# Performance work log

Hardware: AMD Instinct MI355X
Metric: run time of the kernel (lower is better)

## Reference

```python
import jax, jax.numpy as jnp
import numpy as np

B, N, D_IN = 4, 512, 64
D_ATT, D_HID, D_ATT_NUM = 32, 128, 2
A_HID = 64
MASK_CONST = 10000.0


def _mlp2(x, W1, b1, W2, b2):
    # 2-layer MLP (Linear-ReLU-Linear), as built by cfg_Block('mlp', ...)
    return jax.nn.relu(x @ W1 + b1) @ W2 + b2


def setup_inputs() -> dict:
    key = jax.random.key(0)
    ks = jax.random.split(key, 32)
    s = 0.1

    def w(k, shp):
        return (jax.random.normal(k, shp, dtype=jnp.float32) * s)

    inp = {"x": jax.random.normal(ks[0], (B, N, D_IN), dtype=jnp.float32)}
    # key / query / value encoders: 64 -> 128 -> 32
    for i, p in enumerate(["k", "q", "v"]):
        inp[p + "W1"] = w(ks[1 + 2 * i], (D_IN, D_HID)); inp[p + "b1"] = jnp.zeros((D_HID,), jnp.float32)
        inp[p + "W2"] = w(ks[2 + 2 * i], (D_HID, D_ATT)); inp[p + "b2"] = jnp.zeros((D_ATT,), jnp.float32)
    # attention MLP: 2*D_att -> 64 -> D_att_num
    inp["aW1"] = w(ks[7], (2 * D_ATT, A_HID)); inp["ab1"] = jnp.zeros((A_HID,), jnp.float32)
    inp["aW2"] = w(ks[8], (A_HID, D_ATT_NUM)); inp["ab2"] = jnp.zeros((D_ATT_NUM,), jnp.float32)
    # decoders (x and y): 2*D_att -> 128 -> 64, then mu/sig heads 64 -> 1
    for i, p in enumerate(["dx", "dy"]):
        inp[p + "W1"] = w(ks[9 + 2 * i], (2 * D_ATT, D_HID)); inp[p + "b1"] = jnp.zeros((D_HID,), jnp.float32)
        inp[p + "W2"] = w(ks[10 + 2 * i], (D_HID, A_HID)); inp[p + "b2"] = jnp.zeros((A_HID,), jnp.float32)
    for i, p in enumerate(["mx", "sx", "my", "sy"]):
        inp[p + "W"] = w(ks[13 + i], (A_HID, 1)); inp[p + "b"] = jnp.zeros((1,), jnp.float32)
    return inp


def reference(x, kW1, kb1, kW2, kb2, qW1, qb1, qW2, qb2, vW1, vb1, vW2, vb2,
              aW1, ab1, aW2, ab2, dxW1, dxb1, dxW2, dxb2, dyW1, dyb1, dyW2, dyb2,
              mxW, mxb, sxW, sxb, myW, myb, syW, syb):
    k = _mlp2(x, kW1, kb1, kW2, kb2)  # [B,N,D_att]
    q = _mlp2(x, qW1, qb1, qW2, qb2)
    v = _mlp2(x, vW1, vb1, vW2, vb2)

    # z[b,i,j] = cat(k[b,i], q[b,j]); first att layer applied without
    # materializing z: z@aW1 = k@aW1[:D] + q@aW1[D:]
    hk = k @ aW1[:D_ATT]          # [B,N,A_HID]
    hq = q @ aW1[D_ATT:]          # [B,N,A_HID]
    h = jax.nn.relu(hk[:, :, None, :] + hq[:, None, :, :] + ab1)  # [B,N,N,A_HID]
    score = h @ aW2 + ab2          # [B,N,N,D_att_num]

    mask = jnp.eye(N, dtype=x.dtype)[None, :, :, None] * MASK_CONST
    w = jax.nn.sigmoid(score - mask)  # [B,N,N,D_att_num]

    agg0 = jnp.einsum('bij,bjd->bid', w[..., 0], v)
    agg1 = jnp.einsum('bij,bjd->bid', w[..., 1], v)
    c0 = jnp.concatenate([v, agg0], axis=-1)  # [B,N,2*D_att]
    c1 = jnp.concatenate([v, agg1], axis=-1)

    d_x = _mlp2(c0, dxW1, dxb1, dxW2, dxb2)
    mu_x = jnp.squeeze(d_x @ mxW + mxb, -1)                 # [B,N]
    sig_x = jnp.squeeze(jax.nn.softplus(d_x @ sxW + sxb), -1)
    d_y = _mlp2(c1, dyW1, dyb1, dyW2, dyb2)
    mu_y = jnp.squeeze(d_y @ myW + myb, -1)
    sig_y = jnp.squeeze(jax.nn.softplus(d_y @ syW + syb), -1)
    return ((mu_x, sig_x), (mu_y, sig_y))
```

## Files before the change

kernel.cpp:

```cpp
#include <hip/hip_runtime.h>
#include <hip/hip_bf16.h>

#define BB 4
#define NN 512

#define WS_V    0
#define WS_HK   65536
#define WS_HQ   196608
#define WS_AGG  327680

__global__ __launch_bounds__(256) void k_enc(
    const float* __restrict__ x,
    const float* __restrict__ kW1, const float* __restrict__ kb1,
    const float* __restrict__ kW2, const float* __restrict__ kb2,
    const float* __restrict__ qW1, const float* __restrict__ qb1,
    const float* __restrict__ qW2, const float* __restrict__ qb2,
    const float* __restrict__ vW1, const float* __restrict__ vb1,
    const float* __restrict__ vW2, const float* __restrict__ vb2,
    const float* __restrict__ aW1, const float* __restrict__ ab1,
    float* __restrict__ wsf)
{
  const int t = threadIdx.x;
  const int bid = blockIdx.x;
  const int e  = bid >> 8;
  const int r0 = (bid & 255) * 8;

  __shared__ float xs[8][64];
  __shared__ float h1s[8][132];
  __shared__ float encs[8][33];

  const float* W1 = (e == 0) ? kW1 : (e == 1) ? qW1 : vW1;
  const float* b1 = (e == 0) ? kb1 : (e == 1) ? qb1 : vb1;
  const float* W2 = (e == 0) ? kW2 : (e == 1) ? qW2 : vW2;
  const float* b2 = (e == 0) ? kb2 : (e == 1) ? qb2 : vb2;

  {
    float2 f = ((const float2*)x)[(size_t)r0 * 32 + t];
    int m = t * 2;
    xs[m >> 6][m & 63] = f.x;
    xs[(m + 1) >> 6][(m + 1) & 63] = f.y;
  }
  __syncthreads();

  {
    const int h = t & 127, rh = t >> 7;
    float acc[4];
    float bb = b1[h];
    #pragma unroll
    for (int r = 0; r < 4; ++r) acc[r] = bb;
    #pragma unroll 4
    for (int i = 0; i < 64; ++i) {
      float wv = W1[i * 128 + h];
      #pragma unroll
      for (int r = 0; r < 4; ++r) acc[r] = fmaf(xs[rh * 4 + r][i], wv, acc[r]);
    }
    #pragma unroll
    for (int r = 0; r < 4; ++r) h1s[rh * 4 + r][h] = fmaxf(acc[r], 0.f);
  }
  __syncthreads();

  {
    const int row = t >> 5, c = t & 31;
    float a = b2[c];
    #pragma unroll 4
    for (int i = 0; i < 128; ++i)
      a = fmaf(h1s[row][i], W2[i * 32 + c], a);
    if (e == 2) wsf[WS_V + (size_t)(r0 + row) * 32 + c] = a;
    else        encs[row][c] = a;
  }

  if (e != 2) {
    __syncthreads();
    const int h = t & 63, rp = t >> 6;
    float bias = (e == 0) ? ab1[h] : 0.f;
    float s0 = bias, s1 = bias;
    const float* aw = aW1 + (e ? 32 * 64 : 0);
    #pragma unroll 4
    for (int cc = 0; cc < 32; ++cc) {
      float wv = aw[cc * 64 + h];
      s0 = fmaf(encs[rp * 2 + 0][cc], wv, s0);
      s1 = fmaf(encs[rp * 2 + 1][cc], wv, s1);
    }
    float* dst = wsf + (e ? WS_HQ : WS_HK);
    dst[(size_t)(r0 + rp * 2 + 0) * 64 + h] = s0;
    dst[(size_t)(r0 + rp * 2 + 1) * 64 + h] = s1;
  }
}

__global__ __launch_bounds__(256, 4) void k_att(
    const float* __restrict__ v_ws, const float* __restrict__ hk_ws,
    const float* __restrict__ hq_ws, const float* __restrict__ aW2,
    const float* __restrict__ ab2, float* __restrict__ aggh)
{
  const int t = threadIdx.x;
  const int bid = blockIdx.x;
  const int jq = bid & 3;
  const int it = (bid >> 2) & 127;
  const int b  = bid >> 9;
  const int i0 = it * 4;
  const int jbase = jq * 128;

  const int q   = t & 3;
  const int jj1 = (t >> 2) & 15;
  const int ii1 = t >> 6;
  const int ig  = i0 + ii1;

  const int dd  = t & 15;
  const int c2  = (t >> 4) & 1;
  const int jh  = (t >> 5) & 1;
  const int i2  = t >> 6;

  __shared__ float hqs[2][16][68];
  __shared__ float vs[2][16][36];
  __shared__ float ws_w[2][4][20];

  float hk16[16];
  {
    const float4* hkp = (const float4*)(hk_ws + ((size_t)b * NN + ig) * 64 + q * 16);
    #pragma unroll
    for (int m = 0; m < 4; ++m) {
      float4 f = hkp[m];
      hk16[4 * m] = f.x; hk16[4 * m + 1] = f.y;
      hk16[4 * m + 2] = f.z; hk16[4 * m + 3] = f.w;
    }
  }
  float aw0[16], aw1[16];
  {
    const float4* awp = (const float4*)(aW2 + q * 32);
    #pragma unroll
    for (int k = 0; k < 8; ++k) {
      float4 f = awp[k];
      aw0[2 * k] = f.x;     aw1[2 * k] = f.y;
      aw0[2 * k + 1] = f.z; aw1[2 * k + 1] = f.w;
    }
  }
  const float sb0 = ab2[0], sb1 = ab2[1];

  float accx = 0.f, accy = 0.f;
  const bool vload = (t < 128);

  {
    float4 hq_r = *(const float4*)(hq_ws + ((size_t)b * NN + jbase + (t >> 4)) * 64 + (t & 15) * 4);
    *(float4*)(&hqs[0][t >> 4][(t & 15) * 4]) = hq_r;
    if (vload) {
      float4 v_r = *(const float4*)(v_ws + ((size_t)b * NN + jbase + (t >> 3)) * 32 + (t & 7) * 4);
      *(float4*)(&vs[0][t >> 3][(t & 7) * 4]) = v_r;
    }
  }
  __syncthreads();

  int p = 0;
  for (int jt = 0; jt < 8; ++jt) {
    const int j0 = jbase + jt * 16;

    float4 hq_n, v_n;
    if (jt < 7) {
      const int j0n = j0 + 16;
      hq_n = *(const float4*)(hq_ws + ((size_t)b * NN + j0n + (t >> 4)) * 64 + (t & 15) * 4);
      if (vload)
        v_n = *(const float4*)(v_ws + ((size_t)b * NN + j0n + (t >> 3)) * 32 + (t & 7) * 4);
    }

    {
      float s0 = 0.f, s1 = 0.f;
      #pragma unroll
      for (int mc = 0; mc < 4; ++mc) {
        float4 hq4 = *(const float4*)(&hqs[p][jj1][q * 16 + mc * 4]);
        float z;
        z = fmaxf(hk16[4 * mc + 0] + hq4.x, 0.f);
        s0 = fmaf(z, aw0[4 * mc + 0], s0); s1 = fmaf(z, aw1[4 * mc + 0], s1);
        z = fmaxf(hk16[4 * mc + 1] + hq4.y, 0.f);
        s0 = fmaf(z, aw0[4 * mc + 1], s0); s1 = fmaf(z, aw1[4 * mc + 1], s1);
        z = fmaxf(hk16[4 * mc + 2] + hq4.z, 0.f);
        s0 = fmaf(z, aw0[4 * mc + 2], s0); s1 = fmaf(z, aw1[4 * mc + 2], s1);
        z = fmaxf(hk16[4 * mc + 3] + hq4.w, 0.f);
        s0 = fmaf(z, aw0[4 * mc + 3], s0); s1 = fmaf(z, aw1[4 * mc + 3], s1);
      }
      s0 += __shfl_xor(s0, 1); s0 += __shfl_xor(s0, 2);
      s1 += __shfl_xor(s1, 1); s1 += __shfl_xor(s1, 2);
      s0 += sb0; s1 += sb1;
      float sel = (q & 1) ? s1 : s0;
      float w = 1.f / (1.f + __expf(-sel));
      if (ig == j0 + jj1) w = 0.f;
      if (q < 2) ws_w[q][ii1][jj1] = w;
    }
    __syncthreads();

    {
      float4 w4a = *(const float4*)(&ws_w[c2][i2][jh * 8]);
      float4 w4b = *(const float4*)(&ws_w[c2][i2][jh * 8 + 4]);
      const int jb = jh * 8;
      float2 vv;
      vv = *(const float2*)(&vs[p][jb + 0][2 * dd]);
      accx = fmaf(w4a.x, vv.x, accx); accy = fmaf(w4a.x, vv.y, accy);
      vv = *(const float2*)(&vs[p][jb + 1][2 * dd]);
      accx = fmaf(w4a.y, vv.x, accx); accy = fmaf(w4a.y, vv.y, accy);
      vv = *(const float2*)(&vs[p][jb + 2][2 * dd]);
      accx = fmaf(w4a.z, vv.x, accx); accy = fmaf(w4a.z, vv.y, accy);
      vv = *(const float2*)(&vs[p][jb + 3][2 * dd]);
      accx = fmaf(w4a.w, vv.x, accx); accy = fmaf(w4a.w, vv.y, accy);
      vv = *(const float2*)(&vs[p][jb + 4][2 * dd]);
      accx = fmaf(w4b.x, vv.x, accx); accy = fmaf(w4b.x, vv.y, accy);
      vv = *(const float2*)(&vs[p][jb + 5][2 * dd]);
      accx = fmaf(w4b.y, vv.x, accx); accy = fmaf(w4b.y, vv.y, accy);
      vv = *(const float2*)(&vs[p][jb + 6][2 * dd]);
      accx = fmaf(w4b.z, vv.x, accx); accy = fmaf(w4b.z, vv.y, accy);
      vv = *(const float2*)(&vs[p][jb + 7][2 * dd]);
      accx = fmaf(w4b.w, vv.x, accx); accy = fmaf(w4b.w, vv.y, accy);
    }

    if (jt < 7) {
      *(float4*)(&hqs[p ^ 1][t >> 4][(t & 15) * 4]) = hq_n;
      if (vload) *(float4*)(&vs[p ^ 1][t >> 3][(t & 7) * 4]) = v_n;
    }
    __syncthreads();
    p ^= 1;
  }

  accx += __shfl_xor(accx, 32);
  accy += __shfl_xor(accy, 32);
  if (jh == 0) {
    const size_t row = (size_t)b * NN + i0 + i2;
    float2 o; o.x = accx; o.y = accy;
    *(float2*)(&aggh[((size_t)(c2 * 4 + jq) * 2048 + row) * 32 + 2 * dd]) = o;
  }
}

__global__ __launch_bounds__(256) void k_dec(
    const float* __restrict__ v_ws, const float* __restrict__ aggh,
    const float* __restrict__ dxW1, const float* __restrict__ dxb1,
    const float* __restrict__ dxW2, const float* __restrict__ dxb2,
    const float* __restrict__ dyW1, const float* __restrict__ dyb1,
    const float* __restrict__ dyW2, const float* __restrict__ dyb2,
    const float* __restrict__ mxW, const float* __restrict__ mxb,
    const float* __restrict__ sxW, const float* __restrict__ sxb,
    const float* __restrict__ myW, const float* __restrict__ myb,
    const float* __restrict__ syW, const float* __restrict__ syb,
    float* __restrict__ out)
{
  const int t = threadIdx.x;
  const int bid = blockIdx.x;
  const int half = bid & 1;
  const int r0 = (bid >> 1) * 2;

  __shared__ float ccs[2][64];
  __shared__ float h1s[2][132];
  __shared__ float dds[2][64];

  if (t < 128) {
    const float* aggp = aggh + (size_t)half * 4 * 65536;
    int r = t >> 6, i = t & 63;
    size_t row = (size_t)(r0 + r);
    float val;
    if (i < 32) {
      val = v_ws[row * 32 + i];
    } else {
      int o = i - 32;
      val = aggp[row * 32 + o] + aggp[65536 + row * 32 + o]
          + aggp[131072 + row * 32 + o] + aggp[196608 + row * 32 + o];
    }
    ccs[r][i] = val;
  }
  __syncthreads();

  const float* W1 = half ? dyW1 : dxW1;
  const float* b1 = half ? dyb1 : dxb1;
  const float* W2 = half ? dyW2 : dxW2;
  const float* b2 = half ? dyb2 : dxb2;

  {
    const int h = t & 127, r = t >> 7;
    float acc = b1[h];
    #pragma unroll 4
    for (int i = 0; i < 64; ++i)
      acc = fmaf(ccs[r][i], W1[i * 128 + h], acc);
    h1s[r][h] = fmaxf(acc, 0.f);
  }
  __syncthreads();

  if (t < 128) {
    const int r = t >> 6, c = t & 63;
    float a = b2[c];
    #pragma unroll 4
    for (int i = 0; i < 128; ++i)
      a = fmaf(h1s[r][i], W2[i * 64 + c], a);
    dds[r][c] = a;
  }
  __syncthreads();

  {
    const int w = t >> 6, lane = t & 63;
    if (w < 2) {
      const float* mW = half ? myW : mxW;
      const float* sW = half ? syW : sxW;
      const float* mb = half ? myb : mxb;
      const float* sb = half ? syb : sxb;
      float dval = dds[w][lane];
      float pm = dval * mW[lane], ps = dval * sW[lane];
      #pragma unroll
      for (int msk = 32; msk >= 1; msk >>= 1) {
        pm += __shfl_xor(pm, msk);
        ps += __shfl_xor(ps, msk);
      }
      if (lane == 0) {
        float mu = pm + mb[0];
        float z = ps + sb[0];
        float sp = (z > 20.f) ? z : log1pf(__expf(z));
        out[half * 4096 + (r0 + w)] = mu;
        out[half * 4096 + 2048 + (r0 + w)] = sp;
      }
    }
  }
}

extern "C" void kernel_launch(void* const* d_in, const int* in_sizes, int n_in,
                              void* d_out, int out_size, void* d_ws, size_t ws_size,
                              hipStream_t stream) {
  (void)in_sizes; (void)n_in; (void)out_size; (void)ws_size;
  const float* x   = (const float*)d_in[0];
  const float* kW1 = (const float*)d_in[1];  const float* kb1 = (const float*)d_in[2];
  const float* kW2 = (const float*)d_in[3];  const float* kb2 = (const float*)d_in[4];
  const float* qW1 = (const float*)d_in[5];  const float* qb1 = (const float*)d_in[6];
  const float* qW2 = (const float*)d_in[7];  const float* qb2 = (const float*)d_in[8];
  const float* vW1 = (const float*)d_in[9];  const float* vb1 = (const float*)d_in[10];
  const float* vW2 = (const float*)d_in[11]; const float* vb2 = (const float*)d_in[12];
  const float* aW1 = (const float*)d_in[13]; const float* ab1 = (const float*)d_in[14];
  const float* aW2 = (const float*)d_in[15]; const float* ab2 = (const float*)d_in[16];
  const float* dxW1 = (const float*)d_in[17]; const float* dxb1 = (const float*)d_in[18];
  const float* dxW2 = (const float*)d_in[19]; const float* dxb2 = (const float*)d_in[20];
  const float* dyW1 = (const float*)d_in[21]; const float* dyb1 = (const float*)d_in[22];
  const float* dyW2 = (const float*)d_in[23]; const float* dyb2 = (const float*)d_in[24];
  const float* mxW = (const float*)d_in[25]; const float* mxb = (const float*)d_in[26];
  const float* sxW = (const float*)d_in[27]; const float* sxb = (const float*)d_in[28];
  const float* myW = (const float*)d_in[29]; const float* myb = (const float*)d_in[30];
  const float* syW = (const float*)d_in[31]; const float* syb = (const float*)d_in[32];

  float* wsf = (float*)d_ws;
  float* out = (float*)d_out;

  hipLaunchKernelGGL(k_enc, dim3(768), dim3(256), 0, stream,
                     x, kW1, kb1, kW2, kb2, qW1, qb1, qW2, qb2, vW1, vb1, vW2, vb2,
                     aW1, ab1, wsf);
  hipLaunchKernelGGL(k_att, dim3(2048), dim3(256), 0, stream,
                     wsf + WS_V, wsf + WS_HK, wsf + WS_HQ, aW2, ab2,
                     wsf + WS_AGG);
  hipLaunchKernelGGL(k_dec, dim3(2048), dim3(256), 0, stream,
                     wsf + WS_V, wsf + WS_AGG,
                     dxW1, dxb1, dxW2, dxb2, dyW1, dyb1, dyW2, dyb2,
                     mxW, mxb, sxW, sxb, myW, myb, syW, syb, out);
}
```

Baseline: 175.0 us.

## Double j-tile width in attention and process four rows per decoder block

The attention kernel now splits j into two halves instead of four and handles 32 j per tile with two sub-iterations, so there are half as many blocks and barriers per j and half as many partial aggregates to write. The decoder now handles four rows per block, reusing each W1 load across two rows and using all threads. It sums two partials instead of four. Fewer blocks may reduce parallelism, and the larger tiles raise shared memory and register use.

```diff
diff --git a/kernel.cpp b/kernel.cpp
--- a/kernel.cpp
+++ b/kernel.cpp
@@ -94,14 +94,14 @@
 {
   const int t = threadIdx.x;
   const int bid = blockIdx.x;
-  const int jq = bid & 3;
-  const int it = (bid >> 2) & 127;
-  const int b  = bid >> 9;
+  const int jq = bid & 1;
+  const int it = (bid >> 1) & 127;
+  const int b  = bid >> 8;
   const int i0 = it * 4;
-  const int jbase = jq * 128;
+  const int jbase = jq * 256;
 
   const int q   = t & 3;
-  const int jj1 = (t >> 2) & 15;
+  const int jj0 = (t >> 2) & 15;
   const int ii1 = t >> 6;
   const int ig  = i0 + ii1;
 
@@ -110,9 +110,9 @@
   const int jh  = (t >> 5) & 1;
   const int i2  = t >> 6;
 
-  __shared__ float hqs[2][16][68];
-  __shared__ float vs[2][16][36];
-  __shared__ float ws_w[2][4][20];
+  __shared__ float hqs[2][32][68];
+  __shared__ float vs[2][32][36];
+  __shared__ float ws_w[2][4][36];
 
   float hk16[16];
   {
@@ -137,35 +137,39 @@
   const float sb0 = ab2[0], sb1 = ab2[1];
 
   float accx = 0.f, accy = 0.f;
-  const bool vload = (t < 128);
-
-  {
-    float4 hq_r = *(const float4*)(hq_ws + ((size_t)b * NN + jbase + (t >> 4)) * 64 + (t & 15) * 4);
-    *(float4*)(&hqs[0][t >> 4][(t & 15) * 4]) = hq_r;
-    if (vload) {
-      float4 v_r = *(const float4*)(v_ws + ((size_t)b * NN + jbase + (t >> 3)) * 32 + (t & 7) * 4);
-      *(float4*)(&vs[0][t >> 3][(t & 7) * 4]) = v_r;
-    }
+
+  const int hr0 = t >> 4, hc0 = (t & 15) * 4;
+  const int vr0 = t >> 3, vc0 = (t & 7) * 4;
+
+  {
+    float4 a = *(const float4*)(hq_ws + ((size_t)b * NN + jbase + hr0) * 64 + hc0);
+    float4 c = *(const float4*)(hq_ws + ((size_t)b * NN + jbase + 16 + hr0) * 64 + hc0);
+    float4 v = *(const float4*)(v_ws + ((size_t)b * NN + jbase + vr0) * 32 + vc0);
+    *(float4*)(&hqs[0][hr0][hc0]) = a;
+    *(float4*)(&hqs[0][16 + hr0][hc0]) = c;
+    *(float4*)(&vs[0][vr0][vc0]) = v;
   }
   __syncthreads();
 
   int p = 0;
   for (int jt = 0; jt < 8; ++jt) {
-    const int j0 = jbase + jt * 16;
-
-    float4 hq_n, v_n;
+    const int j0 = jbase + jt * 32;
+
+    float4 hq_n0, hq_n1, v_n;
     if (jt < 7) {
-      const int j0n = j0 + 16;
-      hq_n = *(const float4*)(hq_ws + ((size_t)b * NN + j0n + (t >> 4)) * 64 + (t & 15) * 4);
-      if (vload)
-        v_n = *(const float4*)(v_ws + ((size_t)b * NN + j0n + (t >> 3)) * 32 + (t & 7) * 4);
-    }
-
-    {
+      const int j0n = j0 + 32;
+      hq_n0 = *(const float4*)(hq_ws + ((size_t)b * NN + j0n + hr0) * 64 + hc0);
+      hq_n1 = *(const float4*)(hq_ws + ((size_t)b * NN + j0n + 16 + hr0) * 64 + hc0);
+      v_n   = *(const float4*)(v_ws + ((size_t)b * NN + j0n + vr0) * 32 + vc0);
+    }
+
+    #pragma unroll
+    for (int sub = 0; sub < 2; ++sub) {
+      const int jj = jj0 + sub * 16;
       float s0 = 0.f, s1 = 0.f;
       #pragma unroll
       for (int mc = 0; mc < 4; ++mc) {
-        float4 hq4 = *(const float4*)(&hqs[p][jj1][q * 16 + mc * 4]);
+        float4 hq4 = *(const float4*)(&hqs[p][jj][q * 16 + mc * 4]);
         float z;
         z = fmaxf(hk16[4 * mc + 0] + hq4.x, 0.f);
         s0 = fmaf(z, aw0[4 * mc + 0], s0); s1 = fmaf(z, aw1[4 * mc + 0], s1);
@@ -181,37 +185,35 @@
       s0 += sb0; s1 += sb1;
       float sel = (q & 1) ? s1 : s0;
       float w = 1.f / (1.f + __expf(-sel));
-      if (ig == j0 + jj1) w = 0.f;
-      if (q < 2) ws_w[q][ii1][jj1] = w;
+      if (ig == j0 + jj) w = 0.f;
+      if (q < 2) ws_w[q][ii1][jj] = w;
     }
     __syncthreads();
 
     {
-      float4 w4a = *(const float4*)(&ws_w[c2][i2][jh * 8]);
-      float4 w4b = *(const float4*)(&ws_w[c2][i2][jh * 8 + 4]);
-      const int jb = jh * 8;
-      float2 vv;
-      vv = *(const float2*)(&vs[p][jb + 0][2 * dd]);
-      accx = fmaf(w4a.x, vv.x, accx); accy = fmaf(w4a.x, vv.y, accy);
-      vv = *(const float2*)(&vs[p][jb + 1][2 * dd]);
-      accx = fmaf(w4a.y, vv.x, accx); accy = fmaf(w4a.y, vv.y, accy);
-      vv = *(const float2*)(&vs[p][jb + 2][2 * dd]);
-      accx = fmaf(w4a.z, vv.x, accx); accy = fmaf(w4a.z, vv.y, accy);
-      vv = *(const float2*)(&vs[p][jb + 3][2 * dd]);
-      accx = fmaf(w4a.w, vv.x, accx); accy = fmaf(w4a.w, vv.y, accy);
-      vv = *(const float2*)(&vs[p][jb + 4][2 * dd]);
-      accx = fmaf(w4b.x, vv.x, accx); accy = fmaf(w4b.x, vv.y, accy);
-      vv = *(const float2*)(&vs[p][jb + 5][2 * dd]);
-      accx = fmaf(w4b.y, vv.x, accx); accy = fmaf(w4b.y, vv.y, accy);
-      vv = *(const float2*)(&vs[p][jb + 6][2 * dd]);
-      accx = fmaf(w4b.z, vv.x, accx); accy = fmaf(w4b.z, vv.y, accy);
-      vv = *(const float2*)(&vs[p][jb + 7][2 * dd]);
-      accx = fmaf(w4b.w, vv.x, accx); accy = fmaf(w4b.w, vv.y, accy);
+      const int jb = jh * 16;
+      float4 wq[4];
+      #pragma unroll
+      for (int k = 0; k < 4; ++k)
+        wq[k] = *(const float4*)(&ws_w[c2][i2][jb + 4 * k]);
+      #pragma unroll
+      for (int k = 0; k < 4; ++k) {
+        float2 vv;
+        vv = *(const float2*)(&vs[p][jb + 4 * k + 0][2 * dd]);
+        accx = fmaf(wq[k].x, vv.x, accx); accy = fmaf(wq[k].x, vv.y, accy);
+        vv = *(const float2*)(&vs[p][jb + 4 * k + 1][2 * dd]);
+        accx = fmaf(wq[k].y, vv.x, accx); accy = fmaf(wq[k].y, vv.y, accy);
+        vv = *(const float2*)(&vs[p][jb + 4 * k + 2][2 * dd]);
+        accx = fmaf(wq[k].z, vv.x, accx); accy = fmaf(wq[k].z, vv.y, accy);
+        vv = *(const float2*)(&vs[p][jb + 4 * k + 3][2 * dd]);
+        accx = fmaf(wq[k].w, vv.x, accx); accy = fmaf(wq[k].w, vv.y, accy);
+      }
     }
 
     if (jt < 7) {
-      *(float4*)(&hqs[p ^ 1][t >> 4][(t & 15) * 4]) = hq_n;
-      if (vload) *(float4*)(&vs[p ^ 1][t >> 3][(t & 7) * 4]) = v_n;
+      *(float4*)(&hqs[p ^ 1][hr0][hc0]) = hq_n0;
+      *(float4*)(&hqs[p ^ 1][16 + hr0][hc0]) = hq_n1;
+      *(float4*)(&vs[p ^ 1][vr0][vc0]) = v_n;
     }
     __syncthreads();
     p ^= 1;
@@ -222,7 +224,7 @@
   if (jh == 0) {
     const size_t row = (size_t)b * NN + i0 + i2;
     float2 o; o.x = accx; o.y = accy;
-    *(float2*)(&aggh[((size_t)(c2 * 4 + jq) * 2048 + row) * 32 + 2 * dd]) = o;
+    *(float2*)(&aggh[((size_t)(c2 * 2 + jq) * 2048 + row) * 32 + 2 * dd]) = o;
   }
 }
 
@@ -241,23 +243,22 @@
   const int t = threadIdx.x;
   const int bid = blockIdx.x;
   const int half = bid & 1;
-  const int r0 = (bid >> 1) * 2;
-
-  __shared__ float ccs[2][64];
-  __shared__ float h1s[2][132];
-  __shared__ float dds[2][64];
-
-  if (t < 128) {
-    const float* aggp = aggh + (size_t)half * 4 * 65536;
-    int r = t >> 6, i = t & 63;
-    size_t row = (size_t)(r0 + r);
+  const int r0 = (bid >> 1) * 4;
+
+  __shared__ float ccs[4][64];
+  __shared__ float h1s[4][132];
+  __shared__ float dds[4][64];
+
+  {
+    const float* aggp = aggh + (size_t)half * 2 * 65536;
+    const int r = t >> 6, i = t & 63;
+    const size_t row = (size_t)(r0 + r);
     float val;
     if (i < 32) {
       val = v_ws[row * 32 + i];
     } else {
-      int o = i - 32;
-      val = aggp[row * 32 + o] + aggp[65536 + row * 32 + o]
-          + aggp[131072 + row * 32 + o] + aggp[196608 + row * 32 + o];
+      const int o = i - 32;
+      val = aggp[row * 32 + o] + aggp[65536 + row * 32 + o];
     }
     ccs[r][i] = val;
   }
@@ -269,16 +270,20 @@
   const float* b2 = half ? dyb2 : dxb2;
 
   {
-    const int h = t & 127, r = t >> 7;
-    float acc = b1[h];
-    #pragma unroll 4
-    for (int i = 0; i < 64; ++i)
-      acc = fmaf(ccs[r][i], W1[i * 128 + h], acc);
-    h1s[r][h] = fmaxf(acc, 0.f);
-  }
-  __syncthreads();
-
-  if (t < 128) {
+    const int h = t & 127, rh = t >> 7;
+    float a0 = b1[h], a1 = a0;
+    #pragma unroll 4
+    for (int i = 0; i < 64; ++i) {
+      float wv = W1[i * 128 + h];
+      a0 = fmaf(ccs[2 * rh + 0][i], wv, a0);
+      a1 = fmaf(ccs[2 * rh + 1][i], wv, a1);
+    }
+    h1s[2 * rh + 0][h] = fmaxf(a0, 0.f);
+    h1s[2 * rh + 1][h] = fmaxf(a1, 0.f);
+  }
+  __syncthreads();
+
+  {
     const int r = t >> 6, c = t & 63;
     float a = b2[c];
     #pragma unroll 4
@@ -290,25 +295,23 @@
 
   {
     const int w = t >> 6, lane = t & 63;
-    if (w < 2) {
-      const float* mW = half ? myW : mxW;
-      const float* sW = half ? syW : sxW;
-      const float* mb = half ? myb : mxb;
-      const float* sb = half ? syb : sxb;
-      float dval = dds[w][lane];
-      float pm = dval * mW[lane], ps = dval * sW[lane];
-      #pragma unroll
-      for (int msk = 32; msk >= 1; msk >>= 1) {
-        pm += __shfl_xor(pm, msk);
-        ps += __shfl_xor(ps, msk);
-      }
-      if (lane == 0) {
-        float mu = pm + mb[0];
-        float z = ps + sb[0];
-        float sp = (z > 20.f) ? z : log1pf(__expf(z));
-        out[half * 4096 + (r0 + w)] = mu;
-        out[half * 4096 + 2048 + (r0 + w)] = sp;
-      }
+    const float* mW = half ? myW : mxW;
+    const float* sW = half ? syW : sxW;
+    const float* mb = half ? myb : mxb;
+    const float* sb = half ? syb : sxb;
+    float dval = dds[w][lane];
+    float pm = dval * mW[lane], ps = dval * sW[lane];
+    #pragma unroll
+    for (int msk = 32; msk >= 1; msk >>= 1) {
+      pm += __shfl_xor(pm, msk);
+      ps += __shfl_xor(ps, msk);
+    }
+    if (lane == 0) {
+      float mu = pm + mb[0];
+      float z = ps + sb[0];
+      float sp = (z > 20.f) ? z : log1pf(__expf(z));
+      out[half * 4096 + (r0 + w)] = mu;
+      out[half * 4096 + 2048 + (r0 + w)] = sp;
     }
   }
 }
@@ -341,10 +344,10 @@
   hipLaunchKernelGGL(k_enc, dim3(768), dim3(256), 0, stream,
                      x, kW1, kb1, kW2, kb2, qW1, qb1, qW2, qb2, vW1, vb1, vW2, vb2,
                      aW1, ab1, wsf);
-  hipLaunchKernelGGL(k_att, dim3(2048), dim3(256), 0, stream,
+  hipLaunchKernelGGL(k_att, dim3(1024), dim3(256), 0, stream,
                      wsf + WS_V, wsf + WS_HK, wsf + WS_HQ, aW2, ab2,
                      wsf + WS_AGG);
-  hipLaunchKernelGGL(k_dec, dim3(2048), dim3(256), 0, stream,
+  hipLaunchKernelGGL(k_dec, dim3(1024), dim3(256), 0, stream,
                      wsf + WS_V, wsf + WS_AGG,
                      dxW1, dxb1, dxW2, dxb2, dyW1, dyb1, dyW2, dyb2,
                      mxW, mxb, sxW, sxb, myW, myb, syW, syb, out);
```

New measurement: 174.2 us. No clear change (-0.4%).
